# Kernel optimization log

Hardware: AMD Instinct MI355X
Metric: run time of the kernel (lower is better)

The kernel has to match this reference:

```python
import jax, jax.numpy as jnp
import numpy as np
import math

B, T, C = 4, 2048, 1024
NH, D = 16, 64


def setup_inputs() -> dict:
    key = jax.random.key(0)
    ks = jax.random.split(key, 7)
    s = 0.02
    return {
        "x": jax.random.normal(ks[0], (B, T, C), dtype=jnp.float32),
        "W_attn": jax.random.normal(ks[1], (C, 3 * C), dtype=jnp.float32) * s,
        "b_attn": jax.random.normal(ks[2], (3 * C,), dtype=jnp.float32) * s,
        "W_proj": jax.random.normal(ks[3], (C, C), dtype=jnp.float32) * s,
        "b_proj": jax.random.normal(ks[4], (C,), dtype=jnp.float32) * s,
        # bQ/bK emulate mean_Q + std_Q*randn (resampled biases), broadcast over heads
        "bQ": 0.5 + 0.1 * jax.random.normal(ks[5], (NH, D), dtype=jnp.float32),
        "bK": 0.3 + 0.1 * jax.random.normal(ks[6], (NH, D), dtype=jnp.float32),
    }


def reference(x, W_attn, b_attn, W_proj, b_proj, bQ, bK):
    b, t, c = x.shape
    nh, d = bQ.shape
    qkv = x @ W_attn + b_attn                       # [B,T,3C]
    q, k, v = jnp.split(qkv, 3, axis=2)
    # [B,T,C] -> [B,nh,T,d]
    q = q.reshape(b, t, nh, d).transpose(0, 2, 1, 3)
    k = k.reshape(b, t, nh, d).transpose(0, 2, 1, 3)
    v = v.reshape(b, t, nh, d).transpose(0, 2, 1, 3)
    q = q + bQ[None, :, None, :]
    k = k + bK[None, :, None, :]
    scores = jnp.einsum('bhqd,bhkd->bhqk', q, k) / math.sqrt(d)
    causal = jnp.tril(jnp.ones((t, t), dtype=bool))
    scores = jnp.where(causal[None, None], scores, jnp.finfo(scores.dtype).min)
    att = jax.nn.softmax(scores, axis=-1)
    y = jnp.einsum('bhqk,bhkd->bhqd', att, v)       # [B,nh,T,d]
    y = y.transpose(0, 2, 1, 3).reshape(b, t, c)
    out = y @ W_proj + b_proj
    return (out, bQ)
```

## Files before the change

### kernel.cpp

```cpp
#include <hip/hip_runtime.h>
#include <hip/hip_bf16.h>

#define B_  4
#define T_  2048
#define C_  1024
#define NH_ 16
#define D_  64
#define BH_ (B_*NH_)
#define M_  (B_*T_)

typedef __attribute__((ext_vector_type(8))) short short8;
typedef __attribute__((ext_vector_type(4))) short short4v;
typedef __attribute__((ext_vector_type(4))) float f32x4;

#define SC2 0.18033688011112043f

__device__ __forceinline__ ushort f2bf(float f) {
    unsigned u = __float_as_uint(f);
    u += 0x7FFF + ((u >> 16) & 1);
    return (ushort)(u >> 16);
}

__device__ __forceinline__ unsigned cvtpk(float lo, float hi) {
    unsigned r;
    asm("v_cvt_pk_bf16_f32 %0, %1, %2" : "=v"(r) : "v"(lo), "v"(hi));
    return r;
}

__device__ __forceinline__ void gload16(const void* g, void* lds) {
    __builtin_amdgcn_global_load_lds(
        (const __attribute__((address_space(1))) void*)g,
        (__attribute__((address_space(3))) void*)lds, 16, 0, 0);
}

__global__ __launch_bounds__(256) void prepass_kernel(
    const float* __restrict__ x, ushort* __restrict__ Xb,
    const float* __restrict__ Wa, ushort* __restrict__ Wat,
    const float* __restrict__ bQ, float* __restrict__ bqDst)
{
    __shared__ float t[64][65];
    const int bid = blockIdx.x;
    const int tid = threadIdx.x;

    if (bid < 2048) {
        const int n8 = M_*C_/8;
        const int stride = 2048 * 256;
        for (int idx = bid*256 + tid; idx < n8; idx += stride) {
            const float* p = x + (size_t)idx * 8;
            f32x4 a = *(const f32x4*)p;
            f32x4 b = *(const f32x4*)(p + 4);
            union { short8 v; ushort u[8]; } pk;
            #pragma unroll
            for (int j = 0; j < 4; ++j) { pk.u[j] = f2bf(a[j]); pk.u[4+j] = f2bf(b[j]); }
            *(short8*)&Xb[(size_t)idx * 8] = pk.v;
        }
    } else if (bid < 2816) {
        const int tb = bid - 2048;
        const int n0 = (tb % 48) * 64;
        const int k0 = (tb / 48) * 64;
        const int K = C_, N = 3*C_;
        #pragma unroll
        for (int it = 0; it < 16; ++it) {
            const int kr = it*4 + (tid >> 6);
            t[kr][tid & 63] = Wa[(size_t)(k0 + kr) * N + n0 + (tid & 63)];
        }
        __syncthreads();
        const int nr8 = tid >> 3;
        const int kc0 = (tid & 7) * 8;
        #pragma unroll
        for (int j = 0; j < 2; ++j) {
            const int nr = j*32 + nr8;
            union { short8 v; ushort u[8]; } pk;
            #pragma unroll
            for (int e = 0; e < 8; ++e) pk.u[e] = f2bf(t[kc0 + e][nr]);
            *(short8*)&Wat[(size_t)(n0 + nr) * K + k0 + kc0] = pk.v;
        }
    } else {
        for (int i = tid; i < NH_*D_; i += 256) bqDst[i] = bQ[i];
    }
}

__global__ __launch_bounds__(256) void transpose_w_kernel(
    const float* __restrict__ in, ushort* __restrict__ out, int K, int N)
{
    __shared__ float t[64][65];
    const int tid = threadIdx.x;
    const int n0 = blockIdx.x * 64;
    const int k0 = blockIdx.y * 64;
    #pragma unroll
    for (int it = 0; it < 16; ++it) {
        const int kr = it*4 + (tid >> 6);
        t[kr][tid & 63] = in[(size_t)(k0 + kr) * N + n0 + (tid & 63)];
    }
    __syncthreads();
    const int nr8 = tid >> 3;
    const int kc0 = (tid & 7) * 8;
    #pragma unroll
    for (int j = 0; j < 2; ++j) {
        const int nr = j*32 + nr8;
        union { short8 v; ushort u[8]; } pk;
        #pragma unroll
        for (int e = 0; e < 8; ++e) pk.u[e] = f2bf(t[kc0 + e][nr]);
        *(short8*)&out[(size_t)(n0 + nr) * K + k0 + kc0] = pk.v;
    }
}

__global__ __launch_bounds__(256) void gemmqkv_kernel(
    const ushort* __restrict__ A, const ushort* __restrict__ Bt,
    const float* __restrict__ b_attn, const float* __restrict__ bQv,
    const float* __restrict__ bKv,
    ushort* __restrict__ Qb, ushort* __restrict__ Kb, ushort* __restrict__ Vt)
{
    __shared__ ushort SH[8192];

    const int K = C_;
    const int tid  = threadIdx.x;
    const int lane = tid & 63;
    const int w    = tid >> 6;
    const int wr   = w >> 1, wc = w & 1;
    const int l16  = lane & 15, lg = lane >> 4;

    const int bid = blockIdx.x;
    const int xcd = bid & 7;
    const int idx = bid >> 3;
    const int m0  = (xcd*8 + (idx & 7)) * 128;
    const int n0  = (idx >> 3) * 128;

    const int srow = lane >> 2;
    const int scol = (lane & 3) * 8;
    const ushort* aS = A  + (size_t)(m0 + w*32 + srow) * K + scol;
    const ushort* bS = Bt + (size_t)(n0 + w*32 + srow) * K + scol;

    f32x4 acc[4][4] = {};
    const int NT = K >> 5;

    #pragma unroll 1
    for (int t = 0; t < NT; ++t) {
        const int kn = t * 32;
        gload16(aS + kn,                SH + w*1024);
        gload16(aS + (size_t)16*K + kn, SH + w*1024 + 512);
        gload16(bS + kn,                SH + 4096 + w*1024);
        gload16(bS + (size_t)16*K + kn, SH + 4096 + w*1024 + 512);
        __syncthreads();

        short8 af[4], bf[4];
        #pragma unroll
        for (int i = 0; i < 4; ++i) {
            af[i] = *(const short8*)&SH[(wr*64 + i*16 + l16)*32 + lg*8];
            bf[i] = *(const short8*)&SH[4096 + (wc*64 + i*16 + l16)*32 + lg*8];
        }
        #pragma unroll
        for (int mi = 0; mi < 4; ++mi)
            #pragma unroll
            for (int ni = 0; ni < 4; ++ni)
                acc[mi][ni] = __builtin_amdgcn_mfma_f32_16x16x32_bf16(
                    af[mi], bf[ni], acc[mi][ni], 0, 0, 0);
        __syncthreads();
    }

    if (n0 >= 2048) {
        ushort* TL = SH;
        const int bblk  = m0 >> 11;
        const int tcol0 = m0 & 2047;
        const int h0    = (n0 & 1023) >> 6;
        #pragma unroll
        for (int ng = 0; ng < 4; ++ng) {
            if (wc == (ng >> 1)) {
                #pragma unroll
                for (int nj = 0; nj < 2; ++nj) {
                    const int ni   = (ng & 1)*2 + nj;
                    const int crow = nj*16 + l16;
                    const float ba = b_attn[n0 + ng*32 + crow];
                    #pragma unroll
                    for (int mi = 0; mi < 4; ++mi)
                        #pragma unroll
                        for (int r = 0; r < 4; ++r)
                            TL[crow*136 + wr*64 + mi*16 + lg*4 + r] =
                                f2bf(acc[mi][ni][r] + ba);
                }
            }
            __syncthreads();
            {
                const int crow = tid >> 3;
                const int slot = tid & 7;
                const int gnl  = ng*32 + crow;
                const int d = gnl & 63, h = h0 + (gnl >> 6);
                ushort* dst = Vt + ((size_t)(bblk*NH_ + h)*D_ + d)*T_
                              + tcol0 + slot*16;
                *(short8*)dst       = *(const short8*)&TL[crow*136 + slot*16];
                *(short8*)(dst + 8) = *(const short8*)&TL[crow*136 + slot*16 + 8];
            }
            __syncthreads();
        }
    } else {
        #pragma unroll
        for (int ni = 0; ni < 4; ++ni) {
            const int n = n0 + wc*64 + ni*16 + l16;
            const int sec = n >> 10;
            const int nn  = n & 1023;
            const int h = nn >> 6, d = nn & 63;
            const float ba = b_attn[n];
            #pragma unroll
            for (int mi = 0; mi < 4; ++mi) {
                #pragma unroll
                for (int r = 0; r < 4; ++r) {
                    const int m = m0 + wr*64 + mi*16 + lg*4 + r;
                    const int b = m >> 11, t = m & 2047;
                    float v = acc[mi][ni][r] + ba;
                    if (sec == 0) {
                        v = (v + bQv[nn]) * SC2;
                        Qb[((size_t)(b*NH_ + h)*T_ + t)*D_ + d] = f2bf(v);
                    } else {
                        v += bKv[nn];
                        Kb[((size_t)(b*NH_ + h)*T_ + t)*D_ + d] = f2bf(v);
                    }
                }
            }
        }
    }
}

__global__ __launch_bounds__(256) void gemm2_kernel(
    const ushort* __restrict__ A, const ushort* __restrict__ Bt,
    float* __restrict__ outp, const float* __restrict__ b_proj,
    int K, int N)
{
    __shared__ ushort SH[24576];

    const int tid  = threadIdx.x;
    const int lane = tid & 63;
    const int w    = tid >> 6;
    const int wr   = w >> 1, wc = w & 1;
    const int l16  = lane & 15, lg = lane >> 4;

    const int bid = blockIdx.x;
    const int xcd = bid & 7;
    const int idx = bid >> 3;
    const int m0  = (xcd*8 + (idx & 7)) * 128;
    const int n0  = (idx >> 3) * 128;

    const int srow = lane >> 2;
    const int scol = (lane & 3) * 8;
    const ushort* aS = A  + (size_t)(m0 + w*32 + srow) * K + scol;
    const ushort* bS = Bt + (size_t)(n0 + w*32 + srow) * K + scol;

    f32x4 acc[4][4] = {};
    const int NT = K >> 5;

    #define STAGE(tk, bi)                                                     \
        do {                                                                  \
            const int kn_ = (tk) * 32;                                        \
            gload16(aS + kn_,                SH + (bi)*4096 + w*1024);        \
            gload16(aS + (size_t)16*K + kn_, SH + (bi)*4096 + w*1024 + 512);  \
            gload16(bS + kn_,                SH + 12288 + (bi)*4096 + w*1024);\
            gload16(bS + (size_t)16*K + kn_, SH + 12288 + (bi)*4096 + w*1024 + 512);\
        } while (0)

    STAGE(0, 0);
    STAGE(1, 1);
    asm volatile("s_waitcnt vmcnt(4)" ::: "memory");
    __builtin_amdgcn_s_barrier();

    for (int t = 0; t < NT; ++t) {
        const int cur = t % 3;
        if (t + 2 < NT)
            STAGE(t + 2, (t + 2) % 3);

        short8 af[4], bf[4];
        #pragma unroll
        for (int i = 0; i < 4; ++i) {
            af[i] = *(const short8*)&SH[cur*4096 + (wr*64 + i*16 + l16)*32 + lg*8];
            bf[i] = *(const short8*)&SH[12288 + cur*4096 + (wc*64 + i*16 + l16)*32 + lg*8];
        }
        #pragma unroll
        for (int mi = 0; mi < 4; ++mi)
            #pragma unroll
            for (int ni = 0; ni < 4; ++ni)
                acc[mi][ni] = __builtin_amdgcn_mfma_f32_16x16x32_bf16(
                    af[mi], bf[ni], acc[mi][ni], 0, 0, 0);

        if (t + 1 < NT) {
            if (t + 2 < NT)
                asm volatile("s_waitcnt vmcnt(4)" ::: "memory");
            else
                asm volatile("s_waitcnt vmcnt(0)" ::: "memory");
            __builtin_amdgcn_s_barrier();
        }
    }
    #undef STAGE

    #pragma unroll
    for (int ni = 0; ni < 4; ++ni) {
        const int n = n0 + wc*64 + ni*16 + l16;
        const float bp = b_proj[n];
        #pragma unroll
        for (int mi = 0; mi < 4; ++mi)
            #pragma unroll
            for (int r = 0; r < 4; ++r) {
                const int m = m0 + wr*64 + mi*16 + lg*4 + r;
                outp[(size_t)m * N + n] = acc[mi][ni][r] + bp;
            }
    }
}

__global__ __launch_bounds__(256, 5) void attn_kernel(
    const ushort* __restrict__ Qb, const ushort* __restrict__ Kb,
    const ushort* __restrict__ Vt, ushort* __restrict__ y)
{
    __shared__ char lds[2][16384];

    const int tid  = threadIdx.x;
    const int lane = tid & 63;
    const int w    = tid >> 6;
    const int l16  = lane & 15, lg = lane >> 4;
    const int bid  = blockIdx.x;
    const int xcd  = bid & 7;
    const int idx  = bid >> 3;
    const int bh   = (xcd << 3) | (idx & 7);
    const int p    = 31 - (idx >> 3);
    const int b    = bh >> 4, h = bh & 15;
    const size_t kvb = (size_t)bh * T_ * D_;
    const size_t vtb = (size_t)bh * D_ * T_;

    int srow[2], scol[2];
    #pragma unroll
    for (int i = 0; i < 2; ++i) {
        const int l = w*2048 + i*1024 + lane*16;
        const int r = l >> 7;
        const int c = (l & 127) ^ ((r & 7) << 4);
        srow[i] = r; scol[i] = c >> 1;
    }

    const f32x4 z4 = {0.f, 0.f, 0.f, 0.f};

    const int qw = p * 64 + w * 16;

    short8 qf[2];
    #pragma unroll
    for (int c = 0; c < 2; ++c)
        qf[c] = *(const short8*)(Qb + kvb +
                    (size_t)(qw + l16)*D_ + c*32 + lg*8);

    f32x4 o[4] = {};
    float mrow = -1e30f;
    float lrow = 0.f;
    const int nt = p + 1;

    #pragma unroll
    for (int i = 0; i < 2; ++i) {
        gload16(Kb + kvb + (size_t)srow[i]*D_ + scol[i],
                &lds[0][w*2048 + i*1024]);
        gload16(Vt + vtb + (size_t)srow[i]*T_ + scol[i],
                &lds[0][8192 + w*2048 + i*1024]);
    }

    #pragma unroll 1
    for (int t = 0; t < nt; ++t) {
        const int kb = t * 64;
        if (t + 1 < nt) {
            char* Lb = lds[(t + 1) & 1];
            const int kb1 = kb + 64;
            #pragma unroll
            for (int i = 0; i < 2; ++i) {
                gload16(Kb + kvb + (size_t)(kb1 + srow[i])*D_ + scol[i],
                        Lb + w*2048 + i*1024);
                gload16(Vt + vtb + (size_t)srow[i]*T_ + kb1 + scol[i],
                        Lb + 8192 + w*2048 + i*1024);
            }
            asm volatile("s_waitcnt vmcnt(4)" ::: "memory");
        } else {
            asm volatile("s_waitcnt vmcnt(0)" ::: "memory");
        }
        __builtin_amdgcn_s_barrier();

        {
            const char* Lk = lds[t & 1];
            const char* Lv = lds[t & 1] + 8192;

            f32x4 s[4];
            #pragma unroll
            for (int t4 = 0; t4 < 4; ++t4) {
                const int r = t4*16 + l16;
                const int m = (r & 7) << 4;
                const short8 kc0 = *(const short8*)(Lk + r*128 + (( lg*16     ) ^ m));
                const short8 kc1 = *(const short8*)(Lk + r*128 + ((64 + lg*16 ) ^ m));
                s[t4] = __builtin_amdgcn_mfma_f32_16x16x32_bf16(kc0, qf[0], z4,    0, 0, 0);
                s[t4] = __builtin_amdgcn_mfma_f32_16x16x32_bf16(kc1, qf[1], s[t4], 0, 0, 0);
            }

            const bool full = (kb + 63 <= qw);
            float x[4][4];
            #pragma unroll
            for (int t4 = 0; t4 < 4; ++t4)
                #pragma unroll
                for (int r = 0; r < 4; ++r) {
                    float v = s[t4][r];
                    if (!full)
                        v = (kb + t4*16 + lg*4 + r <= qw + l16) ? v : -1e30f;
                    x[t4][r] = v;
                }
            float vm0 = fmaxf(fmaxf(x[0][0], x[0][1]), fmaxf(x[0][2], x[0][3]));
            float vm1 = fmaxf(fmaxf(x[1][0], x[1][1]), fmaxf(x[1][2], x[1][3]));
            float vm2 = fmaxf(fmaxf(x[2][0], x[2][1]), fmaxf(x[2][2], x[2][3]));
            float vm3 = fmaxf(fmaxf(x[3][0], x[3][1]), fmaxf(x[3][2], x[3][3]));
            float vm  = fmaxf(fmaxf(vm0, vm1), fmaxf(vm2, vm3));
            vm = fmaxf(vm, __shfl_xor(vm, 16, 64));
            vm = fmaxf(vm, __shfl_xor(vm, 32, 64));
            const float mn = fmaxf(mrow, vm);
            float rs = 0.f;
            #pragma unroll
            for (int t4 = 0; t4 < 4; ++t4)
                #pragma unroll
                for (int r = 0; r < 4; ++r) {
                    const float pe = __builtin_amdgcn_exp2f(x[t4][r] - mn);
                    x[t4][r] = pe;
                    rs += pe;
                }
            rs += __shfl_xor(rs, 16, 64);
            rs += __shfl_xor(rs, 32, 64);
            if (__all(vm <= mrow)) {
                lrow += rs;
            } else {
                const float al = __builtin_amdgcn_exp2f(mrow - mn);
                lrow = lrow*al + rs;
                #pragma unroll
                for (int cb = 0; cb < 4; ++cb)
                    #pragma unroll
                    for (int r = 0; r < 4; ++r)
                        o[cb][r] *= al;
            }
            mrow = mn;

            union { unsigned u[4]; short8 v; } p0, p1;
            p0.u[0] = cvtpk(x[0][0], x[0][1]);
            p0.u[1] = cvtpk(x[0][2], x[0][3]);
            p0.u[2] = cvtpk(x[1][0], x[1][1]);
            p0.u[3] = cvtpk(x[1][2], x[1][3]);
            p1.u[0] = cvtpk(x[2][0], x[2][1]);
            p1.u[1] = cvtpk(x[2][2], x[2][3]);
            p1.u[2] = cvtpk(x[3][0], x[3][1]);
            p1.u[3] = cvtpk(x[3][2], x[3][3]);

            #pragma unroll
            for (int cb = 0; cb < 4; ++cb) {
                const int d = cb*16 + l16;
                const int mv = (d & 7) << 4;
                const char* vb = Lv + d*128;
                union { short8 v; short4v hh[2]; } v0, v1;
                v0.hh[0] = *(const short4v*)(vb + ((lg*8     ) ^ mv));
                v0.hh[1] = *(const short4v*)(vb + ((lg*8 + 32) ^ mv));
                v1.hh[0] = *(const short4v*)(vb + ((lg*8 + 64) ^ mv));
                v1.hh[1] = *(const short4v*)(vb + ((lg*8 + 96) ^ mv));
                o[cb] = __builtin_amdgcn_mfma_f32_16x16x32_bf16(v0.v, p0.v, o[cb], 0, 0, 0);
                o[cb] = __builtin_amdgcn_mfma_f32_16x16x32_bf16(v1.v, p1.v, o[cb], 0, 0, 0);
            }
        }
        __builtin_amdgcn_s_barrier();
    }

    {
        const float inv = 1.0f / lrow;
        const int q = qw + l16;
        ushort* yr = y + ((size_t)b*T_ + q)*C_ + h*D_ + lg*4;
        #pragma unroll
        for (int cb = 0; cb < 4; ++cb) {
            union { unsigned u[2]; short4v v; } st;
            st.u[0] = cvtpk(o[cb][0]*inv, o[cb][1]*inv);
            st.u[1] = cvtpk(o[cb][2]*inv, o[cb][3]*inv);
            *(short4v*)(yr + cb*16) = st.v;
        }
    }
}

extern "C" void kernel_launch(void* const* d_in, const int* in_sizes, int n_in,
                              void* d_out, int out_size, void* d_ws, size_t ws_size,
                              hipStream_t stream)
{
    const float* x      = (const float*)d_in[0];
    const float* W_attn = (const float*)d_in[1];
    const float* b_attn = (const float*)d_in[2];
    const float* W_proj = (const float*)d_in[3];
    const float* b_proj = (const float*)d_in[4];
    const float* bQ     = (const float*)d_in[5];
    const float* bK     = (const float*)d_in[6];
    float* out = (float*)d_out;

    const size_t HE = (size_t)BH_ * T_ * D_;
    ushort* Qb = (ushort*)d_ws;
    ushort* Kb = Qb + HE;
    ushort* Vt = Kb + HE;
    ushort* y  = Vt + HE;
    ushort* Wpt = (ushort*)d_ws;

    ushort* Xb  = (ushort*)d_out;
    ushort* Wat = (ushort*)d_out + (size_t)M_ * C_;

    prepass_kernel<<<2817, 256, 0, stream>>>(x, Xb, W_attn, Wat,
                                             bQ, out + (size_t)M_ * C_);

    gemmqkv_kernel<<<1536, 256, 0, stream>>>(
        Xb, Wat, b_attn, bQ, bK, Qb, Kb, Vt);

    attn_kernel<<<2048, 256, 0, stream>>>(Qb, Kb, Vt, y);

    transpose_w_kernel<<<dim3(C_/64, C_/64), 256, 0, stream>>>(W_proj, Wpt, C_, C_);

    gemm2_kernel<<<512, 256, 0, stream>>>(
        y, Wpt, out, b_proj, C_, C_);
}
```

Baseline: 218.4 us.

## Enlarge QKV GEMM tile to 128x256 with 8 waves and triple-buffered LDS pipeline

The QKV projection GEMM now uses 512-thread blocks computing 128x256 tiles, which halves the grid and raises reuse of each A tile. The K loop is rewritten with a three-stage LDS ring buffer: loads run two steps ahead and each step uses a single barrier gated by an explicit vmcnt wait, replacing the two full syncthreads per step. The V transpose epilogue is reworked to stage the whole 256-column tile through LDS in one pass. The cost is 72KB of LDS per block, which limits occupancy, and more reliance on hand-tuned waitcnt counts.

```diff
diff --git a/kernel.cpp b/kernel.cpp
--- a/kernel.cpp
+++ b/kernel.cpp
@@ -105,49 +105,58 @@
     }
 }
 
-__global__ __launch_bounds__(256) void gemmqkv_kernel(
+__global__ __launch_bounds__(512) void gemmqkv_kernel(
     const ushort* __restrict__ A, const ushort* __restrict__ Bt,
     const float* __restrict__ b_attn, const float* __restrict__ bQv,
     const float* __restrict__ bKv,
     ushort* __restrict__ Qb, ushort* __restrict__ Kb, ushort* __restrict__ Vt)
 {
-    __shared__ ushort SH[8192];
+    __shared__ ushort SH[36864];
 
     const int K = C_;
     const int tid  = threadIdx.x;
     const int lane = tid & 63;
     const int w    = tid >> 6;
-    const int wr   = w >> 1, wc = w & 1;
+    const int wr   = w >> 2;
+    const int wc   = w & 3;
     const int l16  = lane & 15, lg = lane >> 4;
 
     const int bid = blockIdx.x;
     const int xcd = bid & 7;
     const int idx = bid >> 3;
     const int m0  = (xcd*8 + (idx & 7)) * 128;
-    const int n0  = (idx >> 3) * 128;
-
-    const int srow = lane >> 2;
-    const int scol = (lane & 3) * 8;
-    const ushort* aS = A  + (size_t)(m0 + w*32 + srow) * K + scol;
-    const ushort* bS = Bt + (size_t)(n0 + w*32 + srow) * K + scol;
+    const int n0  = (idx >> 3) * 256;
+
+    const ushort* aBase = A  + (size_t)(m0 + w*16 + (lane >> 2)) * K + (lane & 3)*8;
+    const ushort* bBase = Bt + (size_t)(n0 + w*32 + (lane >> 2)) * K + (lane & 3)*8;
 
     f32x4 acc[4][4] = {};
     const int NT = K >> 5;
 
+    #define STAGE(tk, bi)                                                     \
+        do {                                                                  \
+            const size_t kn_ = (size_t)(tk) * 32;                             \
+            gload16(aBase + kn_,               SH + (bi)*4096 + w*512);       \
+            gload16(bBase + kn_,               SH + 12288 + (bi)*8192 + w*1024); \
+            gload16(bBase + (size_t)16*K + kn_,SH + 12288 + (bi)*8192 + w*1024 + 512); \
+        } while (0)
+
+    STAGE(0, 0);
+    STAGE(1, 1);
+    asm volatile("s_waitcnt vmcnt(3)" ::: "memory");
+    __builtin_amdgcn_s_barrier();
+
     #pragma unroll 1
     for (int t = 0; t < NT; ++t) {
-        const int kn = t * 32;
-        gload16(aS + kn,                SH + w*1024);
-        gload16(aS + (size_t)16*K + kn, SH + w*1024 + 512);
-        gload16(bS + kn,                SH + 4096 + w*1024);
-        gload16(bS + (size_t)16*K + kn, SH + 4096 + w*1024 + 512);
-        __syncthreads();
+        const int cur = t % 3;
+        if (t + 2 < NT)
+            STAGE(t + 2, (t + 2) % 3);
 
         short8 af[4], bf[4];
         #pragma unroll
         for (int i = 0; i < 4; ++i) {
-            af[i] = *(const short8*)&SH[(wr*64 + i*16 + l16)*32 + lg*8];
-            bf[i] = *(const short8*)&SH[4096 + (wc*64 + i*16 + l16)*32 + lg*8];
+            af[i] = *(const short8*)&SH[cur*4096 + (wr*64 + i*16 + l16)*32 + lg*8];
+            bf[i] = *(const short8*)&SH[12288 + cur*8192 + (wc*64 + i*16 + l16)*32 + lg*8];
         }
         #pragma unroll
         for (int mi = 0; mi < 4; ++mi)
@@ -155,44 +164,18 @@
             for (int ni = 0; ni < 4; ++ni)
                 acc[mi][ni] = __builtin_amdgcn_mfma_f32_16x16x32_bf16(
                     af[mi], bf[ni], acc[mi][ni], 0, 0, 0);
-        __syncthreads();
-    }
-
-    if (n0 >= 2048) {
-        ushort* TL = SH;
-        const int bblk  = m0 >> 11;
-        const int tcol0 = m0 & 2047;
-        const int h0    = (n0 & 1023) >> 6;
-        #pragma unroll
-        for (int ng = 0; ng < 4; ++ng) {
-            if (wc == (ng >> 1)) {
-                #pragma unroll
-                for (int nj = 0; nj < 2; ++nj) {
-                    const int ni   = (ng & 1)*2 + nj;
-                    const int crow = nj*16 + l16;
-                    const float ba = b_attn[n0 + ng*32 + crow];
-                    #pragma unroll
-                    for (int mi = 0; mi < 4; ++mi)
-                        #pragma unroll
-                        for (int r = 0; r < 4; ++r)
-                            TL[crow*136 + wr*64 + mi*16 + lg*4 + r] =
-                                f2bf(acc[mi][ni][r] + ba);
-                }
-            }
-            __syncthreads();
-            {
-                const int crow = tid >> 3;
-                const int slot = tid & 7;
-                const int gnl  = ng*32 + crow;
-                const int d = gnl & 63, h = h0 + (gnl >> 6);
-                ushort* dst = Vt + ((size_t)(bblk*NH_ + h)*D_ + d)*T_
-                              + tcol0 + slot*16;
-                *(short8*)dst       = *(const short8*)&TL[crow*136 + slot*16];
-                *(short8*)(dst + 8) = *(const short8*)&TL[crow*136 + slot*16 + 8];
-            }
-            __syncthreads();
-        }
-    } else {
+
+        if (t + 1 < NT) {
+            if (t + 2 < NT)
+                asm volatile("s_waitcnt vmcnt(3)" ::: "memory");
+            else
+                asm volatile("s_waitcnt vmcnt(0)" ::: "memory");
+            __builtin_amdgcn_s_barrier();
+        }
+    }
+    #undef STAGE
+
+    if (n0 < 2048) {
         #pragma unroll
         for (int ni = 0; ni < 4; ++ni) {
             const int n = n0 + wc*64 + ni*16 + l16;
@@ -205,17 +188,45 @@
                 #pragma unroll
                 for (int r = 0; r < 4; ++r) {
                     const int m = m0 + wr*64 + mi*16 + lg*4 + r;
-                    const int b = m >> 11, t = m & 2047;
+                    const int b = m >> 11, tt = m & 2047;
                     float v = acc[mi][ni][r] + ba;
                     if (sec == 0) {
                         v = (v + bQv[nn]) * SC2;
-                        Qb[((size_t)(b*NH_ + h)*T_ + t)*D_ + d] = f2bf(v);
+                        Qb[((size_t)(b*NH_ + h)*T_ + tt)*D_ + d] = f2bf(v);
                     } else {
                         v += bKv[nn];
-                        Kb[((size_t)(b*NH_ + h)*T_ + t)*D_ + d] = f2bf(v);
+                        Kb[((size_t)(b*NH_ + h)*T_ + tt)*D_ + d] = f2bf(v);
                     }
                 }
             }
+        }
+    } else {
+        __syncthreads();
+        ushort* TL = SH;
+        const int bblk  = m0 >> 11;
+        const int tcol0 = m0 & 2047;
+        const int h0    = (n0 & 1023) >> 6;
+        #pragma unroll
+        for (int ni = 0; ni < 4; ++ni) {
+            const int nl = wc*64 + ni*16 + l16;
+            const float ba = b_attn[n0 + nl];
+            #pragma unroll
+            for (int mi = 0; mi < 4; ++mi)
+                #pragma unroll
+                for (int r = 0; r < 4; ++r)
+                    TL[nl*136 + wr*64 + mi*16 + lg*4 + r] =
+                        f2bf(acc[mi][ni][r] + ba);
+        }
+        __syncthreads();
+        #pragma unroll
+        for (int it = 0; it < 4; ++it) {
+            const int row  = it*64 + (tid >> 3);
+            const int slot = tid & 7;
+            const int d = row & 63, h = h0 + (row >> 6);
+            ushort* dst = Vt + ((size_t)(bblk*NH_ + h)*D_ + d)*T_
+                          + tcol0 + slot*16;
+            *(short8*)dst       = *(const short8*)&TL[row*136 + slot*16];
+            *(short8*)(dst + 8) = *(const short8*)&TL[row*136 + slot*16 + 8];
         }
     }
 }
@@ -498,7 +509,7 @@
     prepass_kernel<<<2817, 256, 0, stream>>>(x, Xb, W_attn, Wat,
                                              bQ, out + (size_t)M_ * C_);
 
-    gemmqkv_kernel<<<1536, 256, 0, stream>>>(
+    gemmqkv_kernel<<<768, 512, 0, stream>>>(
         Xb, Wat, b_attn, bQ, bK, Qb, Kb, Vt);
 
     attn_kernel<<<2048, 256, 0, stream>>>(Qb, Kb, Vt, y);
```

After: 183.9 us. -15.8%, faster.
